# Kernel tuning notes

Measured on AMD Instinct MI355X. Metric: run time of the kernel, lower is better.

Reference implementation:

```python
import jax, jax.numpy as jnp
import numpy as np

BN_EPS = 1e-5


def setup_inputs() -> dict:
    key = jax.random.key(0)
    ks = jax.random.split(key, 7)
    B, C, N = 8, 512, 2048
    P = C // 2
    x = jax.random.normal(ks[0], (B, C, N), dtype=jnp.float32)
    # 1x1 conv weights (no bias), shape [out, in]
    Wg = jax.random.normal(ks[1], (P, C), dtype=jnp.float32) * (1.0 / np.sqrt(C))
    Wtheta = jax.random.normal(ks[2], (P, C), dtype=jnp.float32) * (1.0 / np.sqrt(C))
    Wphi = jax.random.normal(ks[3], (P, C), dtype=jnp.float32) * (1.0 / np.sqrt(C))
    Wz = jax.random.normal(ks[4], (C, P), dtype=jnp.float32) * (1.0 / np.sqrt(P))
    gamma = jnp.ones((C,), dtype=jnp.float32)
    beta = jnp.zeros((C,), dtype=jnp.float32)
    return {"x": x, "Wg": Wg, "Wtheta": Wtheta, "Wphi": Wphi, "Wz": Wz,
            "gamma": gamma, "beta": beta}


def reference(x, Wg, Wtheta, Wphi, Wz, gamma, beta):
    # x: [B, C, N]
    g = jnp.einsum('pc,bcn->bnp', Wg, x)        # [B, N, P]
    theta = jnp.einsum('pc,bcn->bnp', Wtheta, x)  # [B, N, P]
    phi = jnp.einsum('pc,bcn->bpn', Wphi, x)      # [B, P, N]
    f = jnp.einsum('bnp,bpm->bnm', theta, phi)    # [B, N, N] unscaled scores
    f = jax.nn.softmax(f, axis=-1)
    y = jnp.einsum('bnm,bmp->bpn', f, g)          # [B, P, N]
    z = jnp.einsum('cp,bpn->bcn', Wz, y)          # [B, C, N]
    # BatchNorm1d (training-mode batch stats over batch and length dims)
    mean = jnp.mean(z, axis=(0, 2), keepdims=True)
    var = jnp.mean((z - mean) ** 2, axis=(0, 2), keepdims=True)
    z_bn = (z - mean) / jnp.sqrt(var + BN_EPS)
    z_bn = z_bn * gamma[None, :, None] + beta[None, :, None]
    return z_bn + x
```

## Files before the change

### kernel.cpp

```cpp
#include <hip/hip_runtime.h>
#include <hip/hip_bf16.h>


typedef __attribute__((ext_vector_type(8))) short short8;
typedef __attribute__((ext_vector_type(4))) float floatx4;

__device__ __forceinline__ unsigned short f2bf(float v) {
    __hip_bfloat16 h = __float2bfloat16(v);
    return *(unsigned short*)&h;
}
__device__ __forceinline__ float bf2f(unsigned short u) {
    __hip_bfloat16 h;
    *(unsigned short*)&h = u;
    return __bfloat162float(h);
}

__global__ __launch_bounds__(256) void transpose_split(
    const float* __restrict__ X, unsigned short* __restrict__ Thi,
    unsigned short* __restrict__ Tlo, int R, int N)
{
    X   += (long)blockIdx.z * R * N;
    Thi += (long)blockIdx.z * N * R;
    Tlo += (long)blockIdx.z * N * R;
    __shared__ float s[32][33];
    const int tx = threadIdx.x & 31, ty = threadIdx.x >> 5;
    const int n0 = blockIdx.x * 32, r0 = blockIdx.y * 32;
#pragma unroll
    for (int r = 0; r < 4; ++r)
        s[ty + r * 8][tx] = X[(long)(r0 + ty + r * 8) * N + n0 + tx];
    __syncthreads();
#pragma unroll
    for (int r = 0; r < 4; ++r) {
        const int n = ty + r * 8;
        const float v = s[tx][n];
        const unsigned short hi = f2bf(v);
        const unsigned short lo = f2bf(v - bf2f(hi));
        Thi[(long)(n0 + n) * R + r0 + tx] = hi;
        Tlo[(long)(n0 + n) * R + r0 + tx] = lo;
    }
}

__global__ __launch_bounds__(256) void split_w2(
    const float* __restrict__ Wth, const float* __restrict__ Wph,
    unsigned short* __restrict__ Whi, unsigned short* __restrict__ Wlo, int PC)
{
    const int i = blockIdx.x * 256 + threadIdx.x;
    if (i < 2 * PC) {
        const float v = (i < PC) ? Wth[i] : Wph[i - PC];
        const unsigned short hi = f2bf(v);
        Whi[i] = hi;
        Wlo[i] = f2bf(v - bf2f(hi));
    }
}

__global__ __launch_bounds__(256) void cast_bf16(
    const float* __restrict__ X, unsigned short* __restrict__ Y)
{
    const long i = ((long)blockIdx.x * 256 + threadIdx.x) * 4;
    const float4 v = *(const float4*)&X[i];
    ushort4 o;
    o.x = f2bf(v.x); o.y = f2bf(v.y); o.z = f2bf(v.z); o.w = f2bf(v.w);
    *(ushort4*)&Y[i] = o;
}

#define BK 32

template <bool SPLIT, int OUTMODE, int FM, int FN>
__global__ __launch_bounds__(256) void mfma_gemm(
    const unsigned short* __restrict__ Ahi, const unsigned short* __restrict__ Alo,
    const unsigned short* __restrict__ Bhi, const unsigned short* __restrict__ Blo,
    void* __restrict__ Cout, void* __restrict__ Cout2,
    int K, int lda, int ldb, int ldc,
    long sA, long sB, long sC,
    float* __restrict__ S1, float* __restrict__ S2)
{
    constexpr int MTM = FM * 32, MTN = FN * 32;
    constexpr int SA = FM / 2, SB = FN / 2;

    Ahi += (long)blockIdx.z * sA;
    Bhi += (long)blockIdx.z * sB;
    if (SPLIT) { Alo += (long)blockIdx.z * sA; Blo += (long)blockIdx.z * sB; }
    float* Cf = (float*)Cout + (long)blockIdx.z * sC;
    unsigned short* Ch = (unsigned short*)Cout + (long)blockIdx.z * sC;
    unsigned short* Cl = (unsigned short*)Cout2 + (long)blockIdx.z * sC;

    __shared__ unsigned short AsH[MTM * BK], BsH[MTN * BK];
    __shared__ unsigned short AsL[SPLIT ? MTM * BK : 8], BsL[SPLIT ? MTN * BK : 8];

    const int tid = threadIdx.x;
    const int wid = tid >> 6, lane = tid & 63;
    const int wm = (wid >> 1) * (FM * 16), wn = (wid & 1) * (FN * 16);
    const int l15 = lane & 15, quad = lane >> 4;
    const int m0 = blockIdx.y * MTM, n0 = blockIdx.x * MTN;

    int arow[SA], acol[SA], brow[SB], bcol[SB];
#pragma unroll
    for (int t = 0; t < SA; ++t) {
        const int gid = t * 256 + tid;
        arow[t] = gid >> 2; acol[t] = (gid & 3) * 8;
    }
#pragma unroll
    for (int t = 0; t < SB; ++t) {
        const int gid = t * 256 + tid;
        brow[t] = gid >> 2; bcol[t] = (gid & 3) * 8;
    }

    short8 pa[SA], pb[SB], paL[SPLIT ? SA : 1], pbL[SPLIT ? SB : 1];

    auto loadTiles = [&](int k0) {
#pragma unroll
        for (int t = 0; t < SA; ++t) {
            const long o = (long)(m0 + arow[t]) * lda + k0 + acol[t];
            pa[t] = *(const short8*)&Ahi[o];
            if (SPLIT) paL[t] = *(const short8*)&Alo[o];
        }
#pragma unroll
        for (int t = 0; t < SB; ++t) {
            const long o = (long)(n0 + brow[t]) * ldb + k0 + bcol[t];
            pb[t] = *(const short8*)&Bhi[o];
            if (SPLIT) pbL[t] = *(const short8*)&Blo[o];
        }
    };
    auto writeTiles = [&]() {
#pragma unroll
        for (int t = 0; t < SA; ++t) {
            *(short8*)&AsH[arow[t] * BK + acol[t]] = pa[t];
            if (SPLIT) *(short8*)&AsL[arow[t] * BK + acol[t]] = paL[t];
        }
#pragma unroll
        for (int t = 0; t < SB; ++t) {
            *(short8*)&BsH[brow[t] * BK + bcol[t]] = pb[t];
            if (SPLIT) *(short8*)&BsL[brow[t] * BK + bcol[t]] = pbL[t];
        }
    };

    floatx4 acc[FM][FN];
#pragma unroll
    for (int i = 0; i < FM; ++i)
#pragma unroll
        for (int j = 0; j < FN; ++j) acc[i][j] = (floatx4){0.f, 0.f, 0.f, 0.f};

    const int iters = K / BK;
    loadTiles(0);
    writeTiles();
    __syncthreads();

    for (int it = 0; it < iters; ++it) {
        if (it + 1 < iters) loadTiles((it + 1) * BK);

        short8 ah[FM], bh[FN], al[SPLIT ? FM : 1], bl[SPLIT ? FN : 1];
#pragma unroll
        for (int i = 0; i < FM; ++i) {
            ah[i] = *(const short8*)&AsH[(wm + i * 16 + l15) * BK + quad * 8];
            if (SPLIT) al[i] = *(const short8*)&AsL[(wm + i * 16 + l15) * BK + quad * 8];
        }
#pragma unroll
        for (int j = 0; j < FN; ++j) {
            bh[j] = *(const short8*)&BsH[(wn + j * 16 + l15) * BK + quad * 8];
            if (SPLIT) bl[j] = *(const short8*)&BsL[(wn + j * 16 + l15) * BK + quad * 8];
        }
#pragma unroll
        for (int i = 0; i < FM; ++i)
#pragma unroll
            for (int j = 0; j < FN; ++j) {
                acc[i][j] = __builtin_amdgcn_mfma_f32_16x16x32_bf16(ah[i], bh[j], acc[i][j], 0, 0, 0);
                if (SPLIT) {
                    acc[i][j] = __builtin_amdgcn_mfma_f32_16x16x32_bf16(ah[i], bl[j], acc[i][j], 0, 0, 0);
                    acc[i][j] = __builtin_amdgcn_mfma_f32_16x16x32_bf16(al[i], bh[j], acc[i][j], 0, 0, 0);
                }
            }

        if (it + 1 < iters) {
            __syncthreads();
            writeTiles();
            __syncthreads();
        }
    }

#pragma unroll
    for (int i = 0; i < FM; ++i)
#pragma unroll
        for (int j = 0; j < FN; ++j) {
            const int m = m0 + wm + i * 16 + quad * 4;
            const int n = n0 + wn + j * 16 + l15;
#pragma unroll
            for (int r = 0; r < 4; ++r) {
                const float v = acc[i][j][r];
                const long idx = (long)(m + r) * ldc + n;
                if (OUTMODE == 0) {
                    Cf[idx] = v;
                } else if (OUTMODE == 1 || OUTMODE == 3) {
                    Ch[idx] = f2bf(v);
                } else {
                    const unsigned short hi = f2bf(v);
                    Ch[idx] = hi;
                    Cl[idx] = f2bf(v - bf2f(hi));
                }
            }
        }

    if (OUTMODE == 3) {
        const int slot = (blockIdx.z * gridDim.x + blockIdx.x) * 2 + (wn >> 6);
#pragma unroll
        for (int i = 0; i < FM; ++i)
#pragma unroll
            for (int r = 0; r < 4; ++r) {
                float s = 0.f, q = 0.f;
#pragma unroll
                for (int j = 0; j < FN; ++j) {
                    const float v = acc[i][j][r];
                    s += v; q += v * v;
                }
#pragma unroll
                for (int msk = 1; msk < 16; msk <<= 1) {
                    s += __shfl_xor(s, msk, 64);
                    q += __shfl_xor(q, msk, 64);
                }
                if (l15 == 0) {
                    const int row = m0 + wm + i * 16 + quad * 4 + r;
                    S1[(long)row * 256 + slot] = s;
                    S2[(long)row * 256 + slot] = q;
                }
            }
    }
}

#define PSTRP 136

__device__ __forceinline__ int swz64(int row, int slot) {
    return (row << 6) + (((slot ^ row) & 7) << 3);
}

__global__ __launch_bounds__(256, 2) void fused_attn(
    const unsigned short* __restrict__ thphH,
    const unsigned short* __restrict__ thphL,
    const unsigned short* __restrict__ gbf,
    float* __restrict__ yp,
    float2* __restrict__ ml)
{
    const int N = 2048, P = 256, P2 = 512;
    const int id = blockIdx.x;
    const int b  = id & 7;
    const int kh = (id >> 3) & 3;
    const int qt = id >> 5;
    const int q0 = qt * 64;

    const unsigned short* thB = thphH + (long)b * N * P2;
    const unsigned short* tlB = thphL + (long)b * N * P2;
    const unsigned short* gB  = gbf   + (long)b * P * N;
    float*  ypB = yp + (long)kh * (8L * N * P) + (long)b * N * P;
    float2* mlB = ml + (long)kh * (8L * N) + (long)b * N;

    __shared__ unsigned short FG[2 * 128 * 64];
    unsigned short* Fh = FG;
    unsigned short* Fl = FG + 128 * 64;
    unsigned short* Gs = FG;
    __shared__ unsigned short Pw[4][16 * PSTRP];
    __shared__ float Aly[64];

    const int tid = threadIdx.x;
    const int wid = tid >> 6, lane = tid & 63;
    const int l15 = lane & 15, quad = lane >> 4;

    short8 tHr[8], tLr[8];
    {
        const unsigned short* t1 = thB + (long)(q0 + wid * 16 + l15) * P2;
        const unsigned short* t2 = tlB + (long)(q0 + wid * 16 + l15) * P2;
#pragma unroll
        for (int kt = 0; kt < 8; ++kt) {
            tHr[kt] = *(const short8*)&t1[kt * 32 + quad * 8];
            tLr[kt] = *(const short8*)&t2[kt * 32 + quad * 8];
        }
    }

    float mrun[4], lrun[4];
#pragma unroll
    for (int r = 0; r < 4; ++r) { mrun[r] = -1e30f; lrun[r] = 0.f; }

    floatx4 oacc[16];
#pragma unroll
    for (int p = 0; p < 16; ++p) oacc[p] = (floatx4){0.f, 0.f, 0.f, 0.f};

    const int prow4 = tid >> 2, lslot = tid & 3;
    short8 pfH[2][2], pfL[2][2];
    short8 pg[2][4];

    for (int mt = 0; mt < 4; ++mt) {
        const int m0 = kh * 512 + mt * 128;

        floatx4 sacc[8];
#pragma unroll
        for (int j = 0; j < 8; ++j) sacc[j] = (floatx4){0.f, 0.f, 0.f, 0.f};

#pragma unroll
        for (int s = 0; s < 2; ++s) {
            const long o = (long)(m0 + s * 64 + prow4) * P2 + P + 0 * 32 + lslot * 8;
            pfH[0][s] = *(const short8*)&thB[o];
            pfL[0][s] = *(const short8*)&tlB[o];
        }
#pragma unroll
        for (int s = 0; s < 2; ++s) {
            const int row = s * 64 + prow4;
            *(short8*)&Fh[swz64(row, lslot)] = pfH[0][s];
            *(short8*)&Fl[swz64(row, lslot)] = pfL[0][s];
        }
#pragma unroll
        for (int s = 0; s < 2; ++s) {
            const long o = (long)(m0 + s * 64 + prow4) * P2 + P + 1 * 32 + lslot * 8;
            pfH[1][s] = *(const short8*)&thB[o];
            pfL[1][s] = *(const short8*)&tlB[o];
        }
        __syncthreads();

#pragma unroll
        for (int kc = 0; kc < 8; ++kc) {
            if (kc < 6) {
#pragma unroll
                for (int s = 0; s < 2; ++s) {
                    const long o = (long)(m0 + s * 64 + prow4) * P2 + P + (kc + 2) * 32 + lslot * 8;
                    pfH[kc & 1][s] = *(const short8*)&thB[o];
                    pfL[kc & 1][s] = *(const short8*)&tlB[o];
                }
            }
            const short8 aH = tHr[kc];
            const short8 aL = tLr[kc];
            const int half = (kc & 1) * 4;
            __builtin_amdgcn_s_setprio(1);
#pragma unroll
            for (int j = 0; j < 8; ++j) {
                const int ro = swz64(j * 16 + l15, half + quad);
                const short8 bh = *(const short8*)&Fh[ro];
                const short8 bl = *(const short8*)&Fl[ro];
                sacc[j] = __builtin_amdgcn_mfma_f32_16x16x32_bf16(aH, bh, sacc[j], 0, 0, 0);
                sacc[j] = __builtin_amdgcn_mfma_f32_16x16x32_bf16(aH, bl, sacc[j], 0, 0, 0);
                sacc[j] = __builtin_amdgcn_mfma_f32_16x16x32_bf16(aL, bh, sacc[j], 0, 0, 0);
            }
            __builtin_amdgcn_s_setprio(0);
            if (kc < 7) {
                const int wh = ((kc + 1) & 1) * 4;
#pragma unroll
                for (int s = 0; s < 2; ++s) {
                    const int row = s * 64 + prow4;
                    *(short8*)&Fh[swz64(row, wh + lslot)] = pfH[(kc + 1) & 1][s];
                    *(short8*)&Fl[swz64(row, wh + lslot)] = pfL[(kc + 1) & 1][s];
                }
            }
            __syncthreads();
        }

        float alpha[4];
#pragma unroll
        for (int r = 0; r < 4; ++r) {
            float v = sacc[0][r];
#pragma unroll
            for (int j = 1; j < 8; ++j) v = fmaxf(v, sacc[j][r]);
            v = fmaxf(v, __shfl_xor(v, 1, 64));
            v = fmaxf(v, __shfl_xor(v, 2, 64));
            v = fmaxf(v, __shfl_xor(v, 4, 64));
            v = fmaxf(v, __shfl_xor(v, 8, 64));
            const float mo = mrun[r];
            const float mn = fmaxf(mo, v);
            mrun[r] = mn;
            alpha[r] = __expf(mo - mn);
        }
        float lpart[4] = {0.f, 0.f, 0.f, 0.f};
#pragma unroll
        for (int j = 0; j < 8; ++j)
#pragma unroll
            for (int r = 0; r < 4; ++r) {
                const float p = __expf(sacc[j][r] - mrun[r]);
                Pw[wid][(quad * 4 + r) * PSTRP + j * 16 + l15] = f2bf(p);
                lpart[r] += p;
            }
#pragma unroll
        for (int r = 0; r < 4; ++r) {
            float s = lpart[r];
            s += __shfl_xor(s, 1, 64);
            s += __shfl_xor(s, 2, 64);
            s += __shfl_xor(s, 4, 64);
            s += __shfl_xor(s, 8, 64);
            lrun[r] = lrun[r] * alpha[r] + s;
        }
        if (l15 == 0) {
#pragma unroll
            for (int r = 0; r < 4; ++r) Aly[wid * 16 + quad * 4 + r] = alpha[r];
        }

#pragma unroll
        for (int s = 0; s < 4; ++s)
            pg[0][s] = *(const short8*)&gB[(long)(s * 64 + prow4) * N + m0 + 0 * 32 + lslot * 8];
#pragma unroll
        for (int s = 0; s < 4; ++s)
            *(short8*)&Gs[swz64(s * 64 + prow4, lslot)] = pg[0][s];
#pragma unroll
        for (int s = 0; s < 4; ++s)
            pg[1][s] = *(const short8*)&gB[(long)(s * 64 + prow4) * N + m0 + 1 * 32 + lslot * 8];
        __syncthreads();

        float alr[4][4];
#pragma unroll
        for (int g = 0; g < 4; ++g)
#pragma unroll
            for (int r = 0; r < 4; ++r) alr[g][r] = Aly[g * 16 + quad * 4 + r];
        int noresc = 1;
#pragma unroll
        for (int g = 0; g < 4; ++g)
#pragma unroll
            for (int r = 0; r < 4; ++r) noresc &= (alr[g][r] == 1.f);
        if (!__all(noresc)) {
#pragma unroll
            for (int g = 0; g < 4; ++g)
#pragma unroll
                for (int pj = 0; pj < 4; ++pj)
#pragma unroll
                    for (int r = 0; r < 4; ++r) oacc[g * 4 + pj][r] *= alr[g][r];
        }

#pragma unroll
        for (int mc = 0; mc < 4; ++mc) {
            if (mc < 2) {
#pragma unroll
                for (int s = 0; s < 4; ++s)
                    pg[mc & 1][s] = *(const short8*)&gB[(long)(s * 64 + prow4) * N + m0 + (mc + 2) * 32 + lslot * 8];
            }
            const int half = (mc & 1) * 4;
            short8 af[4];
#pragma unroll
            for (int g = 0; g < 4; ++g)
                af[g] = *(const short8*)&Pw[g][l15 * PSTRP + mc * 32 + quad * 8];
            __builtin_amdgcn_s_setprio(1);
#pragma unroll
            for (int pj = 0; pj < 4; ++pj) {
                const short8 bg = *(const short8*)&Gs[swz64(wid * 64 + pj * 16 + l15, half + quad)];
#pragma unroll
                for (int g = 0; g < 4; ++g)
                    oacc[g * 4 + pj] = __builtin_amdgcn_mfma_f32_16x16x32_bf16(af[g], bg, oacc[g * 4 + pj], 0, 0, 0);
            }
            __builtin_amdgcn_s_setprio(0);
            if (mc < 3) {
                const int wh = ((mc + 1) & 1) * 4;
#pragma unroll
                for (int s = 0; s < 4; ++s)
                    *(short8*)&Gs[swz64(s * 64 + prow4, wh + lslot)] = pg[(mc + 1) & 1][s];
                __syncthreads();
            }
        }
    }

    if (l15 == 0) {
#pragma unroll
        for (int r = 0; r < 4; ++r) Aly[wid * 16 + quad * 4 + r] = 1.0f / lrun[r];
    }
    __syncthreads();
    float liv[4][4];
#pragma unroll
    for (int g = 0; g < 4; ++g)
#pragma unroll
        for (int r = 0; r < 4; ++r) liv[g][r] = Aly[g * 16 + quad * 4 + r];
#pragma unroll
    for (int g = 0; g < 4; ++g)
#pragma unroll
        for (int pj = 0; pj < 4; ++pj)
#pragma unroll
            for (int r = 0; r < 4; ++r) {
                const int row = q0 + g * 16 + quad * 4 + r;
                const int col = wid * 64 + pj * 16 + l15;
                ypB[(long)row * P + col] = oacc[g * 4 + pj][r] * liv[g][r];
            }
    if (l15 == 0) {
#pragma unroll
        for (int r = 0; r < 4; ++r) {
            const int row = q0 + wid * 16 + quad * 4 + r;
            mlB[row] = float2{mrun[r], lrun[r]};
        }
    }
}

__global__ __launch_bounds__(256) void attn_merge(
    const float* __restrict__ yp, const float2* __restrict__ ml,
    unsigned short* __restrict__ ybf)
{
    const long STRIDE = 8L * 2048 * 256;
    const long NROWS  = 8L * 2048;
    const long t = (long)blockIdx.x * 256 + threadIdx.x;
    const long row = t >> 5;
    const int  c0  = ((int)t & 31) * 8;
    const float2 a0 = ml[row];
    const float2 a1 = ml[NROWS + row];
    const float2 a2 = ml[2 * NROWS + row];
    const float2 a3 = ml[3 * NROWS + row];
    const float mx = fmaxf(fmaxf(a0.x, a1.x), fmaxf(a2.x, a3.x));
    const float w0 = a0.y * __expf(a0.x - mx);
    const float w1 = a1.y * __expf(a1.x - mx);
    const float w2 = a2.y * __expf(a2.x - mx);
    const float w3 = a3.y * __expf(a3.x - mx);
    const float inv = 1.0f / (w0 + w1 + w2 + w3);
    const float f0 = w0 * inv, f1 = w1 * inv, f2 = w2 * inv, f3 = w3 * inv;
    const long base = row * 256 + c0;
    const float4 u0 = *(const float4*)&yp[base];
    const float4 u1 = *(const float4*)&yp[base + 4];
    const float4 v0 = *(const float4*)&yp[STRIDE + base];
    const float4 v1 = *(const float4*)&yp[STRIDE + base + 4];
    const float4 p0 = *(const float4*)&yp[2 * STRIDE + base];
    const float4 p1 = *(const float4*)&yp[2 * STRIDE + base + 4];
    const float4 q0 = *(const float4*)&yp[3 * STRIDE + base];
    const float4 q1 = *(const float4*)&yp[3 * STRIDE + base + 4];
    ushort4 o0, o1;
    o0.x = f2bf(f0 * u0.x + f1 * v0.x + f2 * p0.x + f3 * q0.x);
    o0.y = f2bf(f0 * u0.y + f1 * v0.y + f2 * p0.y + f3 * q0.y);
    o0.z = f2bf(f0 * u0.z + f1 * v0.z + f2 * p0.z + f3 * q0.z);
    o0.w = f2bf(f0 * u0.w + f1 * v0.w + f2 * p0.w + f3 * q0.w);
    o1.x = f2bf(f0 * u1.x + f1 * v1.x + f2 * p1.x + f3 * q1.x);
    o1.y = f2bf(f0 * u1.y + f1 * v1.y + f2 * p1.y + f3 * q1.y);
    o1.z = f2bf(f0 * u1.z + f1 * v1.z + f2 * p1.z + f3 * q1.z);
    o1.w = f2bf(f0 * u1.w + f1 * v1.w + f2 * p1.w + f3 * q1.w);
    *(ushort4*)&ybf[base] = o0;
    *(ushort4*)&ybf[base + 4] = o1;
}

__global__ __launch_bounds__(256) void bn_finalize(
    const float* __restrict__ p1, const float* __restrict__ p2,
    float* __restrict__ mean, float* __restrict__ rstd, float cnt)
{
    const int c = blockIdx.x, t = threadIdx.x;
    __shared__ float rs[256], rq[256];
    rs[t] = p1[(long)c * 256 + t];
    rq[t] = p2[(long)c * 256 + t];
    __syncthreads();
    for (int st = 128; st > 0; st >>= 1) {
        if (t < st) { rs[t] += rs[t + st]; rq[t] += rq[t + st]; }
        __syncthreads();
    }
    if (t == 0) {
        const float m = rs[0] / cnt;
        mean[c] = m;
        rstd[c] = rsqrtf(rq[0] / cnt - m * m + 1e-5f);
    }
}

__global__ __launch_bounds__(256) void bn_apply_bf(
    const unsigned short* __restrict__ z, const float* __restrict__ x,
    const float* __restrict__ mean, const float* __restrict__ rstd,
    const float* __restrict__ gamma, const float* __restrict__ beta,
    float* __restrict__ out, int C, int N)
{
    const long i = ((long)blockIdx.x * 256 + threadIdx.x) * 8;
    const int c = (int)((i / N) % C);
    const float mu = mean[c], rs = rstd[c], ga = gamma[c], be = beta[c];
    const ushort4 z0 = *(const ushort4*)&z[i];
    const ushort4 z1 = *(const ushort4*)&z[i + 4];
    const float4 x0 = *(const float4*)&x[i];
    const float4 x1 = *(const float4*)&x[i + 4];
    float4 o0, o1;
    o0.x = (bf2f(z0.x) - mu) * rs * ga + be + x0.x;
    o0.y = (bf2f(z0.y) - mu) * rs * ga + be + x0.y;
    o0.z = (bf2f(z0.z) - mu) * rs * ga + be + x0.z;
    o0.w = (bf2f(z0.w) - mu) * rs * ga + be + x0.w;
    o1.x = (bf2f(z1.x) - mu) * rs * ga + be + x1.x;
    o1.y = (bf2f(z1.y) - mu) * rs * ga + be + x1.y;
    o1.z = (bf2f(z1.z) - mu) * rs * ga + be + x1.z;
    o1.w = (bf2f(z1.w) - mu) * rs * ga + be + x1.w;
    *(float4*)&out[i] = o0;
    *(float4*)&out[i + 4] = o1;
}

extern "C" void kernel_launch(void* const* d_in, const int* in_sizes, int n_in,
                              void* d_out, int out_size, void* d_ws, size_t ws_size,
                              hipStream_t stream)
{
    const int B = 8, C = 512, N = 2048, P = 256;
    const float* x      = (const float*)d_in[0];
    const float* Wg     = (const float*)d_in[1];
    const float* Wtheta = (const float*)d_in[2];
    const float* Wphi   = (const float*)d_in[3];
    const float* Wz     = (const float*)d_in[4];
    const float* gamma  = (const float*)d_in[5];
    const float* beta   = (const float*)d_in[6];
    float* out = (float*)d_out;

    float* ws = (float*)d_ws;
    const long NCle = (long)N * C;
    const long NP   = (long)N * P;
    const long R0   = (long)B * NCle;
    unsigned short* xtH   = (unsigned short*)ws;
    unsigned short* xtL   = xtH + B * NCle;
    unsigned short* zbf   = (unsigned short*)ws;
    unsigned short* thphH = (unsigned short*)(ws + R0);
    unsigned short* thphL = thphH + B * NCle;
    unsigned short* gbf   = (unsigned short*)(ws + 2 * R0);
    unsigned short* fbf   = gbf + B * NP;
    unsigned short* ybf   = fbf + (long)B * N * N;
    unsigned short* W2H   = ybf + B * NP;
    unsigned short* W2L   = W2H + 2L * P * C;
    unsigned short* WgB   = W2L + 2L * P * C;
    unsigned short* WzB   = WgB + (long)P * C;
    float*          yp    = (float*)fbf;
    float2*         ml    = (float2*)(ws + 6L * 1024 * 1024);
    float*          bnp1  = ws + R0;
    float*          bnp2  = bnp1 + (long)C * 256;
    float*          mean  = bnp2 + (long)C * 256;
    float*          rstd  = mean + C;

    const long sX = (long)C * N;
    const int  P2 = 2 * P;

    transpose_split<<<dim3(N / 32, C / 32, B), 256, 0, stream>>>(x, xtH, xtL, C, N);
    split_w2<<<(2 * P * C + 255) / 256, 256, 0, stream>>>(Wtheta, Wphi, W2H, W2L, P * C);
    cast_bf16<<<P * C / 1024, 256, 0, stream>>>(Wg, WgB);
    cast_bf16<<<P * C / 1024, 256, 0, stream>>>(Wz, WzB);

    mfma_gemm<true, 2, 4, 4><<<dim3(P2 / 128, N / 128, B), 256, 0, stream>>>(
        xtH, xtL, W2H, W2L, thphH, thphL, C, C, C, P2, NCle, 0, NCle, nullptr, nullptr);
    mfma_gemm<false, 1, 2, 4><<<dim3(N / 128, P / 64, B), 256, 0, stream>>>(
        WgB, WgB, xtH, xtH, gbf, gbf, C, C, C, N, 0, NCle, NP, nullptr, nullptr);

    fused_attn<<<dim3(1024), 256, 0, stream>>>(thphH, thphL, gbf, yp, ml);
    attn_merge<<<dim3(2048), 256, 0, stream>>>(yp, ml, ybf);

    mfma_gemm<false, 3, 4, 4><<<dim3(N / 128, C / 128, B), 256, 0, stream>>>(
        WzB, WzB, ybf, ybf, zbf, zbf, P, P, P, N, 0, NP, sX, bnp1, bnp2);

    bn_finalize<<<C, 256, 0, stream>>>(bnp1, bnp2, mean, rstd, (float)B * N);
    bn_apply_bf<<<(int)((B * sX) / 2048), 256, 0, stream>>>(zbf, x, mean, rstd, gamma, beta, out, C, N);
}
```

Baseline: 281.7 us.

## Use direct global-to-LDS double-buffered loads in GEMM and halve attention key splits

The GEMM kernel now stages tiles with global_load_lds straight into double-buffered shared memory, which removes the register round-trip and one barrier per iteration. Separately, the fused attention kernel splits the key dimension two ways instead of four, so it launches 512 blocks that each loop over 8 key tiles. The merge kernel then combines two partials instead of four, which cuts partial-output traffic. In exchange, attention parallelism drops to 512 blocks and GEMM LDS usage doubles, which may lower occupancy.

```diff
diff --git a/kernel.cpp b/kernel.cpp
--- a/kernel.cpp
+++ b/kernel.cpp
@@ -13,6 +13,12 @@
     __hip_bfloat16 h;
     *(unsigned short*)&h = u;
     return __bfloat162float(h);
+}
+
+__device__ __forceinline__ void gl16(const unsigned short* g, unsigned short* l) {
+    __builtin_amdgcn_global_load_lds(
+        (const __attribute__((address_space(1))) unsigned int*)g,
+        (__attribute__((address_space(3))) unsigned int*)l, 16, 0, 0);
 }
 
 __global__ __launch_bounds__(256) void transpose_split(
@@ -76,6 +82,7 @@
 {
     constexpr int MTM = FM * 32, MTN = FN * 32;
     constexpr int SA = FM / 2, SB = FN / 2;
+    constexpr int ASZ = MTM * BK, BSZ = MTN * BK;
 
     Ahi += (long)blockIdx.z * sA;
     Bhi += (long)blockIdx.z * sB;
@@ -84,8 +91,8 @@
     unsigned short* Ch = (unsigned short*)Cout + (long)blockIdx.z * sC;
     unsigned short* Cl = (unsigned short*)Cout2 + (long)blockIdx.z * sC;
 
-    __shared__ unsigned short AsH[MTM * BK], BsH[MTN * BK];
-    __shared__ unsigned short AsL[SPLIT ? MTM * BK : 8], BsL[SPLIT ? MTN * BK : 8];
+    __shared__ unsigned short AsH[2 * ASZ], BsH[2 * BSZ];
+    __shared__ unsigned short AsL[SPLIT ? 2 * ASZ : 8], BsL[SPLIT ? 2 * BSZ : 8];
 
     const int tid = threadIdx.x;
     const int wid = tid >> 6, lane = tid & 63;
@@ -105,34 +112,22 @@
         brow[t] = gid >> 2; bcol[t] = (gid & 3) * 8;
     }
 
-    short8 pa[SA], pb[SB], paL[SPLIT ? SA : 1], pbL[SPLIT ? SB : 1];
-
-    auto loadTiles = [&](int k0) {
+    auto stage = [&](int k0, int buf) {
 #pragma unroll
         for (int t = 0; t < SA; ++t) {
             const long o = (long)(m0 + arow[t]) * lda + k0 + acol[t];
-            pa[t] = *(const short8*)&Ahi[o];
-            if (SPLIT) paL[t] = *(const short8*)&Alo[o];
+            const int d = buf * ASZ + (t * 256 + tid) * 8;
+            gl16(&Ahi[o], &AsH[d]);
+            if (SPLIT) gl16(&Alo[o], &AsL[d]);
         }
 #pragma unroll
         for (int t = 0; t < SB; ++t) {
             const long o = (long)(n0 + brow[t]) * ldb + k0 + bcol[t];
-            pb[t] = *(const short8*)&Bhi[o];
-            if (SPLIT) pbL[t] = *(const short8*)&Blo[o];
+            const int d = buf * BSZ + (t * 256 + tid) * 8;
+            gl16(&Bhi[o], &BsH[d]);
+            if (SPLIT) gl16(&Blo[o], &BsL[d]);
         }
     };
-    auto writeTiles = [&]() {
-#pragma unroll
-        for (int t = 0; t < SA; ++t) {
-            *(short8*)&AsH[arow[t] * BK + acol[t]] = pa[t];
-            if (SPLIT) *(short8*)&AsL[arow[t] * BK + acol[t]] = paL[t];
-        }
-#pragma unroll
-        for (int t = 0; t < SB; ++t) {
-            *(short8*)&BsH[brow[t] * BK + bcol[t]] = pb[t];
-            if (SPLIT) *(short8*)&BsL[brow[t] * BK + bcol[t]] = pbL[t];
-        }
-    };
 
     floatx4 acc[FM][FN];
 #pragma unroll
@@ -141,23 +136,23 @@
         for (int j = 0; j < FN; ++j) acc[i][j] = (floatx4){0.f, 0.f, 0.f, 0.f};
 
     const int iters = K / BK;
-    loadTiles(0);
-    writeTiles();
+    stage(0, 0);
     __syncthreads();
 
     for (int it = 0; it < iters; ++it) {
-        if (it + 1 < iters) loadTiles((it + 1) * BK);
+        const int cur = it & 1;
+        if (it + 1 < iters) stage((it + 1) * BK, cur ^ 1);
 
         short8 ah[FM], bh[FN], al[SPLIT ? FM : 1], bl[SPLIT ? FN : 1];
 #pragma unroll
         for (int i = 0; i < FM; ++i) {
-            ah[i] = *(const short8*)&AsH[(wm + i * 16 + l15) * BK + quad * 8];
-            if (SPLIT) al[i] = *(const short8*)&AsL[(wm + i * 16 + l15) * BK + quad * 8];
+            ah[i] = *(const short8*)&AsH[cur * ASZ + (wm + i * 16 + l15) * BK + quad * 8];
+            if (SPLIT) al[i] = *(const short8*)&AsL[cur * ASZ + (wm + i * 16 + l15) * BK + quad * 8];
         }
 #pragma unroll
         for (int j = 0; j < FN; ++j) {
-            bh[j] = *(const short8*)&BsH[(wn + j * 16 + l15) * BK + quad * 8];
-            if (SPLIT) bl[j] = *(const short8*)&BsL[(wn + j * 16 + l15) * BK + quad * 8];
+            bh[j] = *(const short8*)&BsH[cur * BSZ + (wn + j * 16 + l15) * BK + quad * 8];
+            if (SPLIT) bl[j] = *(const short8*)&BsL[cur * BSZ + (wn + j * 16 + l15) * BK + quad * 8];
         }
 #pragma unroll
         for (int i = 0; i < FM; ++i)
@@ -170,11 +165,7 @@
                 }
             }
 
-        if (it + 1 < iters) {
-            __syncthreads();
-            writeTiles();
-            __syncthreads();
-        }
+        __syncthreads();
     }
 
 #pragma unroll
@@ -241,8 +232,8 @@
     const int N = 2048, P = 256, P2 = 512;
     const int id = blockIdx.x;
     const int b  = id & 7;
-    const int kh = (id >> 3) & 3;
-    const int qt = id >> 5;
+    const int kh = (id >> 3) & 1;
+    const int qt = id >> 4;
     const int q0 = qt * 64;
 
     const unsigned short* thB = thphH + (long)b * N * P2;
@@ -285,8 +276,8 @@
     short8 pfH[2][2], pfL[2][2];
     short8 pg[2][4];
 
-    for (int mt = 0; mt < 4; ++mt) {
-        const int m0 = kh * 512 + mt * 128;
+    for (int mt = 0; mt < 8; ++mt) {
+        const int m0 = kh * 1024 + mt * 128;
 
         floatx4 sacc[8];
 #pragma unroll
@@ -480,40 +471,31 @@
     const float* __restrict__ yp, const float2* __restrict__ ml,
     unsigned short* __restrict__ ybf)
 {
-    const long STRIDE = 8L * 2048 * 256;
-    const long NROWS  = 8L * 2048;
+    const long HALF = 8L * 2048 * 256;
     const long t = (long)blockIdx.x * 256 + threadIdx.x;
     const long row = t >> 5;
     const int  c0  = ((int)t & 31) * 8;
-    const float2 a0 = ml[row];
-    const float2 a1 = ml[NROWS + row];
-    const float2 a2 = ml[2 * NROWS + row];
-    const float2 a3 = ml[3 * NROWS + row];
-    const float mx = fmaxf(fmaxf(a0.x, a1.x), fmaxf(a2.x, a3.x));
-    const float w0 = a0.y * __expf(a0.x - mx);
-    const float w1 = a1.y * __expf(a1.x - mx);
-    const float w2 = a2.y * __expf(a2.x - mx);
-    const float w3 = a3.y * __expf(a3.x - mx);
-    const float inv = 1.0f / (w0 + w1 + w2 + w3);
-    const float f0 = w0 * inv, f1 = w1 * inv, f2 = w2 * inv, f3 = w3 * inv;
+    const float2 a = ml[row];
+    const float2 c = ml[8L * 2048 + row];
+    const float mx = fmaxf(a.x, c.x);
+    const float w1 = a.y * __expf(a.x - mx);
+    const float w2 = c.y * __expf(c.x - mx);
+    const float inv = 1.0f / (w1 + w2);
+    const float f1 = w1 * inv, f2 = w2 * inv;
     const long base = row * 256 + c0;
     const float4 u0 = *(const float4*)&yp[base];
     const float4 u1 = *(const float4*)&yp[base + 4];
-    const float4 v0 = *(const float4*)&yp[STRIDE + base];
-    const float4 v1 = *(const float4*)&yp[STRIDE + base + 4];
-    const float4 p0 = *(const float4*)&yp[2 * STRIDE + base];
-    const float4 p1 = *(const float4*)&yp[2 * STRIDE + base + 4];
-    const float4 q0 = *(const float4*)&yp[3 * STRIDE + base];
-    const float4 q1 = *(const float4*)&yp[3 * STRIDE + base + 4];
+    const float4 v0 = *(const float4*)&yp[HALF + base];
+    const float4 v1 = *(const float4*)&yp[HALF + base + 4];
     ushort4 o0, o1;
-    o0.x = f2bf(f0 * u0.x + f1 * v0.x + f2 * p0.x + f3 * q0.x);
-    o0.y = f2bf(f0 * u0.y + f1 * v0.y + f2 * p0.y + f3 * q0.y);
-    o0.z = f2bf(f0 * u0.z + f1 * v0.z + f2 * p0.z + f3 * q0.z);
-    o0.w = f2bf(f0 * u0.w + f1 * v0.w + f2 * p0.w + f3 * q0.w);
-    o1.x = f2bf(f0 * u1.x + f1 * v1.x + f2 * p1.x + f3 * q1.x);
-    o1.y = f2bf(f0 * u1.y + f1 * v1.y + f2 * p1.y + f3 * q1.y);
-    o1.z = f2bf(f0 * u1.z + f1 * v1.z + f2 * p1.z + f3 * q1.z);
-    o1.w = f2bf(f0 * u1.w + f1 * v1.w + f2 * p1.w + f3 * q1.w);
+    o0.x = f2bf(f1 * u0.x + f2 * v0.x);
+    o0.y = f2bf(f1 * u0.y + f2 * v0.y);
+    o0.z = f2bf(f1 * u0.z + f2 * v0.z);
+    o0.w = f2bf(f1 * u0.w + f2 * v0.w);
+    o1.x = f2bf(f1 * u1.x + f2 * v1.x);
+    o1.y = f2bf(f1 * u1.y + f2 * v1.y);
+    o1.z = f2bf(f1 * u1.z + f2 * v1.z);
+    o1.w = f2bf(f1 * u1.w + f2 * v1.w);
     *(ushort4*)&ybf[base] = o0;
     *(ushort4*)&ybf[base + 4] = o1;
 }
@@ -614,7 +596,7 @@
     mfma_gemm<false, 1, 2, 4><<<dim3(N / 128, P / 64, B), 256, 0, stream>>>(
         WgB, WgB, xtH, xtH, gbf, gbf, C, C, C, N, 0, NCle, NP, nullptr, nullptr);
 
-    fused_attn<<<dim3(1024), 256, 0, stream>>>(thphH, thphL, gbf, yp, ml);
+    fused_attn<<<dim3(512), 256, 0, stream>>>(thphH, thphL, gbf, yp, ml);
     attn_merge<<<dim3(2048), 256, 0, stream>>>(yp, ml, ybf);
 
     mfma_gemm<false, 3, 4, 4><<<dim3(N / 128, C / 128, B), 256, 0, stream>>>(
```

Measured after the change: 266.9 us. 5.3% less time.
